# Optimization experiments

Hardware: AMD Instinct MI355X
Metric: run time of the kernel (lower is better)

## Reference

```python
import jax, jax.numpy as jnp
import numpy as np

B, T, D = 32, 512, 768
PROJ, HID, NL, VOCAB = 50, 409, 4, 17


def setup_inputs() -> dict:
    key = jax.random.key(0)
    ks = jax.random.split(key, 10)
    s = 0.05
    return {
        "enc": jax.random.normal(ks[0], (B, T, D), jnp.float32),
        "W_proj": jax.random.normal(ks[1], (PROJ, D), jnp.float32) * s,
        "Wih": jax.random.normal(ks[2], (NL, 2, 4 * HID, 2 * HID), jnp.float32) * s,
        "Whh": jax.random.normal(ks[3], (NL, 2, 4 * HID, HID), jnp.float32) * s,
        "bih": jax.random.normal(ks[4], (NL, 2, 4 * HID), jnp.float32) * s,
        "bhh": jax.random.normal(ks[5], (NL, 2, 4 * HID), jnp.float32) * s,
        "W1": jax.random.normal(ks[6], (512, 2 * HID), jnp.float32) * s,
        "b1": jax.random.normal(ks[7], (512,), jnp.float32) * s,
        "W2": jax.random.normal(ks[8], (VOCAB, 512), jnp.float32) * s,
        "b2": jax.random.normal(ks[9], (VOCAB,), jnp.float32) * s,
    }


def _ngram_pool(enc):
    # width-3 sliding mean; token 0 averages tokens [0:2]; last token is itself.
    b, t, d = enc.shape
    pad = jnp.pad(enc, ((0, 0), (1, 1), (0, 0)))
    ssum = pad[:, :-2] + pad[:, 1:-1] + pad[:, 2:]          # [B,T,D]
    cnt = jnp.full((t,), 3.0, enc.dtype).at[0].set(2.0)
    ng = ssum / cnt[None, :, None]
    return ng.at[:, -1].set(enc[:, -1])                      # last = mean of single token


def _lstm_dir(x, Wih, Whh, bih, bhh, reverse):
    # x: [T,B,in] -> hidden states [T,B,HID]; PyTorch gate order i,f,g,o.
    pre = jnp.einsum('tbi,gi->tbg', x, Wih) + bih + bhh     # [T,B,4H]
    bsz = x.shape[1]
    h0 = jnp.zeros((bsz, HID), x.dtype)

    def step(carry, p):
        h, c = carry
        g = p + h @ Whh.T
        i, f, gg, o = jnp.split(g, 4, axis=-1)
        c = jax.nn.sigmoid(f) * c + jax.nn.sigmoid(i) * jnp.tanh(gg)
        h = jax.nn.sigmoid(o) * jnp.tanh(c)
        return (h, c), h

    _, hs = jax.lax.scan(step, (h0, h0), pre, reverse=reverse)
    return hs


def reference(enc, W_proj, Wih, Whh, bih, bhh, W1, b1, W2, b2):
    ng = _ngram_pool(enc)                                    # [B,T,768]
    proj = ng @ W_proj.T                                     # [B,T,50]
    h = jnp.concatenate([enc, proj], axis=-1)                # [B,T,818]
    x = jnp.swapaxes(h, 0, 1)                                # [T,B,818]
    for l in range(NL):
        fwd = _lstm_dir(x, Wih[l, 0], Whh[l, 0], bih[l, 0], bhh[l, 0], False)
        bwd = _lstm_dir(x, Wih[l, 1], Whh[l, 1], bih[l, 1], bhh[l, 1], True)
        x = jnp.concatenate([fwd, bwd], axis=-1)             # [T,B,818]
    out = jnp.swapaxes(x, 0, 1)                              # [B,T,818]
    # fc: Linear -> Dropout(eval: identity) -> Linear
    logits = (out @ W1.T + b1) @ W2.T + b2                   # [B,T,17]
    return logits
```

## Files before the change

### kernel.cpp

```cpp
#include <hip/hip_runtime.h>
#include <stdint.h>


typedef __attribute__((ext_vector_type(8))) short bf16x8;
typedef __attribute__((ext_vector_type(4))) float f32x4;
typedef unsigned short u16;
typedef unsigned int u32;

constexpr int kT = 512, kB = 32, kDIN = 768, kPROJ = 50;
constexpr int kHID = 409, kKH = 416, kNG = 1664, kXD = 832;
constexpr int kM = kT * kB;
constexpr int kH4 = 1636;
constexpr int kIN = 818;

#define MFMA_B16(acc, a, b) \
  acc = __builtin_amdgcn_mfma_f32_16x16x32_bf16(a, b, acc, 0, 0, 0)

__device__ __forceinline__ u16 f2bf(float x) {
  uint32_t u = __float_as_uint(x);
  uint32_t r = (u + 0x7FFFu + ((u >> 16) & 1u)) >> 16;
  return (u16)r;
}
__device__ __forceinline__ float bf2f(u16 v) {
  return __uint_as_float(((uint32_t)v) << 16);
}
__device__ __forceinline__ float sigm(float x) { return 1.f / (1.f + __expf(-x)); }
__device__ __forceinline__ float tanh_(float x) { return 1.f - 2.f / (__expf(2.f * x) + 1.f); }

__device__ __forceinline__ void cload(bf16x8& d, const u16* p) {
  asm volatile("global_load_dwordx4 %0, %1, off sc0 sc1" : "=v"(d) : "v"(p) : "memory");
}
__device__ __forceinline__ u32 cload_u32(const u32* p) {
  u32 v;
  asm volatile("global_load_dword %0, %1, off sc0 sc1\n\ts_waitcnt vmcnt(0)"
               : "=v"(v) : "v"(p) : "memory");
  return v;
}
__device__ __forceinline__ void cstore_u32(u32* p, u32 v) {
  asm volatile("global_store_dword %0, %1, off sc0 sc1" :: "v"(p), "v"(v) : "memory");
}

__global__ void pack_wih_k(int layer, const float* __restrict__ Wsrc,
                           u16* __restrict__ wh, u16* __restrict__ wl) {
  const size_t total = (size_t)2 * kNG * kXD;
  for (size_t i = (size_t)blockIdx.x * blockDim.x + threadIdx.x; i < total;
       i += (size_t)gridDim.x * blockDim.x) {
    int k = (int)(i % kXD);
    size_t r1 = i / kXD;
    int row = (int)(r1 % kNG);
    int d = (int)(r1 / kNG);
    int g = row / kKH, j = row % kKH;
    float v = 0.f;
    if (j < kHID && k < kIN)
      v = Wsrc[((size_t)(layer * 2 + d) * kH4 + g * kHID + j) * kIN + k];
    u16 hb = f2bf(v);
    wh[i] = hb;
    wl[i] = f2bf(v - bf2f(hb));
  }
}

__global__ void pack_whh_k(int layer, const float* __restrict__ Wsrc,
                           u16* __restrict__ wh, u16* __restrict__ wl) {
  const size_t total = (size_t)2 * kNG * kKH;
  for (size_t i = (size_t)blockIdx.x * blockDim.x + threadIdx.x; i < total;
       i += (size_t)gridDim.x * blockDim.x) {
    int k = (int)(i % kKH);
    size_t r1 = i / kKH;
    int row = (int)(r1 % kNG);
    int d = (int)(r1 / kNG);
    int g = row / kKH, j = row % kKH;
    float v = 0.f;
    if (j < kHID && k < kHID)
      v = Wsrc[((size_t)(layer * 2 + d) * kH4 + g * kHID + j) * kHID + k];
    u16 hb = f2bf(v);
    wh[i] = hb;
    wl[i] = f2bf(v - bf2f(hb));
  }
}

__global__ void pack_bias_k(const float* __restrict__ bih,
                            const float* __restrict__ bhh,
                            float* __restrict__ bias) {
  int i = blockIdx.x * 256 + threadIdx.x;
  if (i >= 8 * kNG) return;
  int row = i % kNG, ld = i / kNG;
  int g = row / kKH, j = row % kKH;
  float v = 0.f;
  if (j < kHID) v = bih[ld * kH4 + g * kHID + j] + bhh[ld * kH4 + g * kHID + j];
  bias[i] = v;
}

__global__ void fold_fc_k(const float* __restrict__ W1, const float* __restrict__ b1,
                          const float* __restrict__ W2, const float* __restrict__ b2,
                          float* __restrict__ wfc, float* __restrict__ bfc) {
  int i = blockIdx.x * 256 + threadIdx.x;
  if (i >= 17 * kXD) return;
  int o = i / kXD, n = i % kXD;
  float s = 0.f;
  if (n < kIN) {
    for (int k = 0; k < 512; ++k) s += W2[o * 512 + k] * W1[(size_t)k * kIN + n];
  }
  wfc[i] = s;
  if (n == 0) {
    float bs = b2[o];
    for (int k = 0; k < 512; ++k) bs += W2[o * 512 + k] * b1[k];
    bfc[o] = bs;
  }
}

__global__ __launch_bounds__(256) void prep_k(const float* __restrict__ enc,
                                              const float* __restrict__ Wp,
                                              u16* __restrict__ x_h,
                                              u16* __restrict__ x_l,
                                              u16* __restrict__ y_h,
                                              u16* __restrict__ y_l) {
  const int t = blockIdx.x >> 2;
  const int b0 = (blockIdx.x & 3) * 8;
  const int tid = threadIdx.x;
  __shared__ __align__(16) float ng_s[8][kDIN];

  for (int idx = tid; idx < 8 * kDIN; idx += 256) {
    int bi = idx / kDIN, c = idx % kDIN;
    int b = b0 + bi;
    float e1 = enc[((size_t)b * kT + t) * kDIN + c];
    float ngv;
    if (t == 0)
      ngv = (e1 + enc[((size_t)b * kT + 1) * kDIN + c]) * 0.5f;
    else if (t == kT - 1)
      ngv = e1;
    else
      ngv = (enc[((size_t)b * kT + t - 1) * kDIN + c] + e1 +
             enc[((size_t)b * kT + t + 1) * kDIN + c]) * (1.f / 3.f);
    ng_s[bi][c] = ngv;
    size_t xo = ((size_t)t * kB + b) * kXD + c;
    u16 hb = f2bf(e1);
    x_h[xo] = hb;
    x_l[xo] = f2bf(e1 - bf2f(hb));
  }
  for (int idx = tid; idx < 8 * (kXD - kIN); idx += 256) {
    int bi = idx / (kXD - kIN), c = kIN + idx % (kXD - kIN);
    size_t xo = ((size_t)t * kB + b0 + bi) * kXD + c;
    x_h[xo] = 0; x_l[xo] = 0;
    y_h[xo] = 0; y_l[xo] = 0;
  }
  __syncthreads();

  const int w = tid >> 6, l_ = tid & 63;
  for (int p = w; p < kPROJ; p += 4) {
    float a0 = 0, a1 = 0, a2 = 0, a3 = 0, a4 = 0, a5 = 0, a6 = 0, a7 = 0;
    for (int j = l_; j < kDIN; j += 64) {
      float wv = Wp[(size_t)p * kDIN + j];
      a0 += wv * ng_s[0][j]; a1 += wv * ng_s[1][j];
      a2 += wv * ng_s[2][j]; a3 += wv * ng_s[3][j];
      a4 += wv * ng_s[4][j]; a5 += wv * ng_s[5][j];
      a6 += wv * ng_s[6][j]; a7 += wv * ng_s[7][j];
    }
    float acc8[8] = {a0, a1, a2, a3, a4, a5, a6, a7};
#pragma unroll
    for (int bi = 0; bi < 8; ++bi) {
      float v = acc8[bi];
      for (int off = 32; off > 0; off >>= 1) v += __shfl_down(v, off);
      if (l_ == 0) {
        size_t xo = ((size_t)t * kB + b0 + bi) * kXD + kDIN + p;
        u16 hb = f2bf(v);
        x_h[xo] = hb;
        x_l[xo] = f2bf(v - bf2f(hb));
      }
    }
  }
}

__global__ __launch_bounds__(256) void gemm_pre_k(
    const u16* __restrict__ Ah, const u16* __restrict__ Al,
    const u16* __restrict__ Bh, const u16* __restrict__ Bl,
    const float* __restrict__ bias, float* __restrict__ C,
    int m_base, int mtShift) {
  __shared__ __align__(16) u16 As_h[128 * 64], As_l[128 * 64];
  __shared__ __align__(16) u16 Bs_h[64 * 64], Bs_l[64 * 64];
  const int tid = threadIdx.x;
  const int l_ = tid & 63, w = tid >> 6;
  const int nt = blockIdx.x >> mtShift;
  const int mt = blockIdx.x & ((1 << mtShift) - 1);
  const int m0 = mt * 128, n0 = nt * 64;
  const int wr = (w & 1) * 64, wc = (w >> 1) * 32;

  f32x4 acc[4][2];
#pragma unroll
  for (int i = 0; i < 4; ++i)
#pragma unroll
    for (int j = 0; j < 2; ++j) acc[i][j] = f32x4{0.f, 0.f, 0.f, 0.f};

  for (int kt = 0; kt < 13; ++kt) {
    const int k0 = kt * 64;
#pragma unroll
    for (int i = 0; i < 4; ++i) {
      int ch = i * 256 + tid;
      int r = ch >> 3, kc = ch & 7;
      const size_t ga = (size_t)(m_base + m0 + r) * kXD + k0 + kc * 8;
      int dst = r * 64 + ((kc ^ (r & 7)) << 3);
      *(int4*)&As_h[dst] = *(const int4*)&Ah[ga];
      *(int4*)&As_l[dst] = *(const int4*)&Al[ga];
    }
#pragma unroll
    for (int i = 0; i < 2; ++i) {
      int ch = i * 256 + tid;
      int r = ch >> 3, kc = ch & 7;
      const size_t gb = (size_t)(n0 + r) * kXD + k0 + kc * 8;
      int dst = r * 64 + ((kc ^ (r & 7)) << 3);
      *(int4*)&Bs_h[dst] = *(const int4*)&Bh[gb];
      *(int4*)&Bs_l[dst] = *(const int4*)&Bl[gb];
    }
    __syncthreads();
#pragma unroll
    for (int ks = 0; ks < 2; ++ks) {
      bf16x8 a_h[4], a_l[4], b_h[2], b_l[2];
#pragma unroll
      for (int mi = 0; mi < 4; ++mi) {
        int r = wr + mi * 16 + (l_ & 15);
        int kc = ks * 4 + (l_ >> 4);
        int ad = r * 64 + ((kc ^ (r & 7)) << 3);
        a_h[mi] = *(const bf16x8*)&As_h[ad];
        a_l[mi] = *(const bf16x8*)&As_l[ad];
      }
#pragma unroll
      for (int ni = 0; ni < 2; ++ni) {
        int r = wc + ni * 16 + (l_ & 15);
        int kc = ks * 4 + (l_ >> 4);
        int ad = r * 64 + ((kc ^ (r & 7)) << 3);
        b_h[ni] = *(const bf16x8*)&Bs_h[ad];
        b_l[ni] = *(const bf16x8*)&Bs_l[ad];
      }
#pragma unroll
      for (int mi = 0; mi < 4; ++mi)
#pragma unroll
        for (int ni = 0; ni < 2; ++ni) {
          MFMA_B16(acc[mi][ni], a_h[mi], b_h[ni]);
          MFMA_B16(acc[mi][ni], a_h[mi], b_l[ni]);
          MFMA_B16(acc[mi][ni], a_l[mi], b_h[ni]);
        }
    }
    __syncthreads();
  }
#pragma unroll
  for (int mi = 0; mi < 4; ++mi)
#pragma unroll
    for (int ni = 0; ni < 2; ++ni) {
      int n = n0 + wc + ni * 16 + (l_ & 15);
      float bv = bias[n];
#pragma unroll
      for (int q = 0; q < 4; ++q) {
        int m = m0 + wr + mi * 16 + (l_ >> 4) * 4 + q;
        C[(size_t)m * kNG + n] = acc[mi][ni][q] + bv;
      }
    }
}

__global__ __launch_bounds__(256) void scan_k(
    int st0, int nsteps, const float* __restrict__ pre,
    const u16* __restrict__ whhH, const u16* __restrict__ whhL,
    u16* __restrict__ xo_h, u16* __restrict__ xo_l,
    u32* __restrict__ h_hi, u32* __restrict__ h_lo,
    float* __restrict__ c_glob, u32* __restrict__ layerFlags) {
  const int tid = threadIdx.x, l_ = tid & 63, w = tid >> 6;
  const int d = blockIdx.x & 1, s = blockIdx.x >> 1;
  const int mt = w & 1, nt2 = w >> 1;

  __shared__ __align__(16) u16 whh_s[2][64][424];
  __shared__ __align__(16) float gate_s[64][33];

  for (int idx = tid; idx < 64 * kKH; idx += 256) {
    int r = idx / kKH, k = idx % kKH;
    int g = r >> 4, j = r & 15;
    size_t src = ((size_t)d * kNG + g * kKH + s * 16 + j) * kKH + k;
    whh_s[0][r][k] = whhH[src];
    whh_s[1][r][k] = whhL[src];
  }

  const int ub = tid >> 3;
  const int uu = tid & 7;
  const int hid0 = s * 16 + 2 * uu;
  float c0 = 0.f, c1 = 0.f;
  if (st0 != 0) {
    c0 = c_glob[(d * 32 + ub) * kKH + hid0];
    c1 = c_glob[(d * 32 + ub) * kKH + hid0 + 1];
  }

  const int arow = mt * 16 + (l_ & 15);
  const int kq = (l_ >> 4) * 8;
  const int lr0 = nt2 * 32 + (l_ & 15);
  const int lr1 = nt2 * 32 + 16 + (l_ & 15);
  const int bq = mt * 16 + (l_ >> 4) * 4;
  const int n0g = (lr0 >> 4) * kKH + s * 16 + (lr0 & 15);
  const int n1g = (lr1 >> 4) * kKH + s * 16 + (lr1 & 15);
  const float* pre_d = pre + (size_t)d * ((size_t)nsteps * kB) * kNG;
  u32* flg = layerFlags + (size_t)d * kT * 32;

  __syncthreads();

  float preg[2][4];
  {
    int lt = d ? (nsteps - 1) : 0;
    const float* p = pre_d + ((size_t)lt * kB + bq) * kNG;
#pragma unroll
    for (int q = 0; q < 4; ++q) {
      preg[0][q] = p[(size_t)q * kNG + n0g];
      preg[1][q] = p[(size_t)q * kNG + n1g];
    }
  }

  for (int stl = 0; stl < nsteps; ++stl) {
    const int st = st0 + stl;
    const int teff = d ? (kT - 1 - st) : st;
    f32x4 acc0, acc1;
#pragma unroll
    for (int q = 0; q < 4; ++q) { acc0[q] = preg[0][q]; acc1[q] = preg[1][q]; }

    if (st > 0) {
      u32* fst = flg + (size_t)(st - 1) * 32;
      if (w == 0 && l_ < 26) {
        int guard = 0;
        while (cload_u32(fst + l_) == 0u) {
          __builtin_amdgcn_s_sleep(1);
          if (++guard > (1 << 20)) break;
        }
      }
      __syncthreads();
      const int slot = st & 1;
      const u16* hh = (const u16*)h_hi + (size_t)(slot * 2 + d) * kB * kKH;
      const u16* hl = (const u16*)h_lo + (size_t)(slot * 2 + d) * kB * kKH;
      bf16x8 ah[13], al[13];
#pragma unroll
      for (int ks = 0; ks < 13; ++ks) {
        cload(ah[ks], hh + arow * kKH + ks * 32 + kq);
        cload(al[ks], hl + arow * kKH + ks * 32 + kq);
      }
      asm volatile("s_waitcnt vmcnt(0)" ::: "memory");
      __builtin_amdgcn_sched_barrier(0);
#pragma unroll
      for (int ks = 0; ks < 13; ++ks) {
        bf16x8 bh0 = *(const bf16x8*)&whh_s[0][lr0][ks * 32 + kq];
        bf16x8 bl0 = *(const bf16x8*)&whh_s[1][lr0][ks * 32 + kq];
        bf16x8 bh1 = *(const bf16x8*)&whh_s[0][lr1][ks * 32 + kq];
        bf16x8 bl1 = *(const bf16x8*)&whh_s[1][lr1][ks * 32 + kq];
        MFMA_B16(acc0, ah[ks], bh0);
        MFMA_B16(acc0, ah[ks], bl0);
        MFMA_B16(acc0, al[ks], bh0);
        MFMA_B16(acc1, ah[ks], bh1);
        MFMA_B16(acc1, ah[ks], bl1);
        MFMA_B16(acc1, al[ks], bh1);
      }
    }

    if (stl + 1 < nsteps) {
      int lt = d ? (nsteps - 2 - stl) : (stl + 1);
      const float* p = pre_d + ((size_t)lt * kB + bq) * kNG;
#pragma unroll
      for (int q = 0; q < 4; ++q) {
        preg[0][q] = p[(size_t)q * kNG + n0g];
        preg[1][q] = p[(size_t)q * kNG + n1g];
      }
    }

#pragma unroll
    for (int q = 0; q < 4; ++q) {
      gate_s[lr0][bq + q] = acc0[q];
      gate_s[lr1][bq + q] = acc1[q];
    }
    __syncthreads();

    {
      int j0 = 2 * uu, j1 = 2 * uu + 1;
      float gi0 = gate_s[0 + j0][ub], gf0 = gate_s[16 + j0][ub];
      float gc0 = gate_s[32 + j0][ub], go0 = gate_s[48 + j0][ub];
      float gi1 = gate_s[0 + j1][ub], gf1 = gate_s[16 + j1][ub];
      float gc1 = gate_s[32 + j1][ub], go1 = gate_s[48 + j1][ub];
      c0 = sigm(gf0) * c0 + sigm(gi0) * tanh_(gc0);
      c1 = sigm(gf1) * c1 + sigm(gi1) * tanh_(gc1);
      float h0v = sigm(go0) * tanh_(c0);
      float h1v = sigm(go1) * tanh_(c1);

      u16 hb0 = f2bf(h0v), lb0 = f2bf(h0v - bf2f(hb0));
      u16 hb1 = f2bf(h1v), lb1 = f2bf(h1v - bf2f(hb1));
      const int outslot = (st + 1) & 1;
      u32 vh = (u32)hb0 | ((u32)hb1 << 16);
      u32 vl = (u32)lb0 | ((u32)lb1 << 16);
      size_t hw = ((size_t)(outslot * 2 + d) * kB + ub) * (kKH / 2) + (hid0 >> 1);
      cstore_u32(h_hi + hw, vh);
      cstore_u32(h_lo + hw, vl);
      if (hid0 < kHID) {
        size_t xo = ((size_t)teff * kB + ub) * kXD + d * kHID + hid0;
        xo_h[xo] = hb0;
        xo_l[xo] = lb0;
        if (hid0 + 1 < kHID) {
          xo_h[xo + 1] = hb1;
          xo_l[xo + 1] = lb1;
        }
      }
    }
    asm volatile("s_waitcnt vmcnt(0)" ::: "memory");
    __syncthreads();
    if (tid == 0) cstore_u32(flg + (size_t)st * 32 + s, 1u);
  }

  c_glob[(d * 32 + ub) * kKH + hid0] = c0;
  c_glob[(d * 32 + ub) * kKH + hid0 + 1] = c1;
}

__global__ __launch_bounds__(128) void fc_k(const u16* __restrict__ x_h,
                                            const u16* __restrict__ x_l,
                                            const float* __restrict__ wfc,
                                            const float* __restrict__ bfc,
                                            float* __restrict__ out) {
  const int m = blockIdx.x;
  const int t = m >> 5, b = m & 31;
  const int tid = threadIdx.x;
  __shared__ __align__(16) float xr[kXD];
  for (int i = tid; i < kXD; i += 128)
    xr[i] = bf2f(x_h[(size_t)m * kXD + i]) + bf2f(x_l[(size_t)m * kXD + i]);
  __syncthreads();
  const int w = tid >> 6, l_ = tid & 63;
  for (int o = w; o < 17; o += 2) {
    float acc = 0.f;
    for (int j = l_; j < kXD; j += 64) acc += xr[j] * wfc[(size_t)o * kXD + j];
    for (int off = 32; off > 0; off >>= 1) acc += __shfl_down(acc, off);
    if (l_ == 0) out[((size_t)b * kT + t) * 17 + o] = acc + bfc[o];
  }
}

extern "C" void kernel_launch(void* const* d_in, const int* in_sizes, int n_in,
                              void* d_out, int out_size, void* d_ws, size_t ws_size,
                              hipStream_t stream) {
  (void)in_sizes; (void)n_in; (void)out_size;
  const float* enc = (const float*)d_in[0];
  const float* Wp  = (const float*)d_in[1];
  const float* Wih = (const float*)d_in[2];
  const float* Whh = (const float*)d_in[3];
  const float* bih = (const float*)d_in[4];
  const float* bhh = (const float*)d_in[5];
  const float* W1  = (const float*)d_in[6];
  const float* b1  = (const float*)d_in[7];
  const float* W2  = (const float*)d_in[8];
  const float* b2  = (const float*)d_in[9];
  float* out = (float*)d_out;

  char* ws = (char*)d_ws;
  size_t off = 0;
  auto alloc = [&](size_t bytes) -> char* {
    char* p = ws + off;
    off += (bytes + 255) & ~(size_t)255;
    return p;
  };
  u16* x0_h  = (u16*)alloc((size_t)kM * kXD * 2);
  u16* x0_l  = (u16*)alloc((size_t)kM * kXD * 2);
  u16* x1_h  = (u16*)alloc((size_t)kM * kXD * 2);
  u16* x1_l  = (u16*)alloc((size_t)kM * kXD * 2);
  u16* wih_h = (u16*)alloc((size_t)2 * kNG * kXD * 2);
  u16* wih_l = (u16*)alloc((size_t)2 * kNG * kXD * 2);
  u16* whh_h = (u16*)alloc((size_t)2 * kNG * kKH * 2);
  u16* whh_l = (u16*)alloc((size_t)2 * kNG * kKH * 2);
  float* bias = (float*)alloc((size_t)8 * kNG * 4);
  u32* h_hi  = (u32*)alloc((size_t)2 * 2 * kB * kKH * 2);
  u32* h_lo  = (u32*)alloc((size_t)2 * 2 * kB * kKH * 2);
  float* c_glob = (float*)alloc((size_t)2 * kB * kKH * 4);
  u32* flags = (u32*)alloc((size_t)4 * 2 * kT * 32 * 4);
  float* wfc = (float*)alloc((size_t)17 * kXD * 4);
  float* bfc = (float*)alloc(32 * 4);

  int TC = 0;
  {
    const int cand[7] = {512, 256, 128, 64, 32, 16, 8};
    for (int i = 0; i < 7; ++i) {
      size_t preB = (size_t)2 * cand[i] * kB * kNG * 4;
      if (off + preB <= ws_size) { TC = cand[i]; break; }
    }
  }
  if (TC == 0) return;
  float* pre = (float*)alloc((size_t)2 * TC * kB * kNG * 4);
  const int mtShift = __builtin_ctz(TC / 4);
  const int nChunks = kT / TC;

  hipMemsetAsync(flags, 0, (size_t)4 * 2 * kT * 32 * 4, stream);

  pack_bias_k<<<dim3(52), dim3(256), 0, stream>>>(bih, bhh, bias);
  fold_fc_k<<<dim3(56), dim3(256), 0, stream>>>(W1, b1, W2, b2, wfc, bfc);
  prep_k<<<dim3(kT * 4), dim3(256), 0, stream>>>(enc, Wp, x0_h, x0_l, x1_h, x1_l);

  for (int l = 0; l < 4; ++l) {
    const bool even = (l & 1) == 0;
    const u16* xi_h = even ? x0_h : x1_h;
    const u16* xi_l = even ? x0_l : x1_l;
    u16* xo_h = even ? x1_h : x0_h;
    u16* xo_l = even ? x1_l : x0_l;

    pack_wih_k<<<dim3(2048), dim3(256), 0, stream>>>(l, Wih, wih_h, wih_l);
    pack_whh_k<<<dim3(1024), dim3(256), 0, stream>>>(l, Whh, whh_h, whh_l);
    for (int c = 0; c < nChunks; ++c) {
      const int st0 = c * TC;
      for (int dd = 0; dd < 2; ++dd) {
        const int m_base = (dd == 0 ? st0 : (kT - st0 - TC)) * kB;
        gemm_pre_k<<<dim3(26 << mtShift), dim3(256), 0, stream>>>(
            xi_h, xi_l, wih_h + (size_t)dd * kNG * kXD,
            wih_l + (size_t)dd * kNG * kXD, bias + (size_t)(l * 2 + dd) * kNG,
            pre + (size_t)dd * TC * kB * kNG, m_base, mtShift);
      }
      scan_k<<<dim3(52), dim3(256), 0, stream>>>(
          st0, TC, pre, whh_h, whh_l, xo_h, xo_l, h_hi, h_lo, c_glob,
          flags + (size_t)l * 2 * kT * 32);
    }
  }
  fc_k<<<dim3(kM), dim3(128), 0, stream>>>(x0_h, x0_l, wfc, bfc, out);
}
```

Baseline: 12.84 ms.

## Overlap h-state loads with MFMA and move non-critical stores off recurrence path

The recurrent LSTM step now waits on the h-state loads in three stages (vmcnt 18/8/0), so MFMAs on early k-slices start while later slices are still arriving. The x-output stores and the next-step preactivation prefetch move after the completion flag is published, which shortens the critical path between dependent steps. The spin-wait drops its s_sleep to cut polling latency, and the input-projection GEMM switches to direct global-to-LDS loads with the swizzle applied on the global side. In exchange, the spin loop polls harder, and the partial vmcnt waits rely on a particular load issue order.

```diff
diff --git a/kernel.cpp b/kernel.cpp
--- a/kernel.cpp
+++ b/kernel.cpp
@@ -38,6 +38,12 @@
 }
 __device__ __forceinline__ void cstore_u32(u32* p, u32 v) {
   asm volatile("global_store_dword %0, %1, off sc0 sc1" :: "v"(p), "v"(v) : "memory");
+}
+
+__device__ __forceinline__ void gload_lds16(const u16* g, u16* l) {
+  __builtin_amdgcn_global_load_lds(
+      (const __attribute__((address_space(1))) unsigned int*)g,
+      (__attribute__((address_space(3))) unsigned int*)l, 16, 0, 0);
 }
 
 __global__ void pack_wih_k(int layer, const float* __restrict__ Wsrc,
@@ -194,21 +200,21 @@
     const int k0 = kt * 64;
 #pragma unroll
     for (int i = 0; i < 4; ++i) {
-      int ch = i * 256 + tid;
-      int r = ch >> 3, kc = ch & 7;
-      const size_t ga = (size_t)(m_base + m0 + r) * kXD + k0 + kc * 8;
-      int dst = r * 64 + ((kc ^ (r & 7)) << 3);
-      *(int4*)&As_h[dst] = *(const int4*)&Ah[ga];
-      *(int4*)&As_l[dst] = *(const int4*)&Al[ga];
+      int slot = i * 256 + tid;
+      int r = slot >> 3, kc = slot & 7;
+      int kcs = kc ^ (r & 7);
+      const size_t ga = (size_t)(m_base + m0 + r) * kXD + k0 + kcs * 8;
+      gload_lds16(Ah + ga, &As_h[slot * 8]);
+      gload_lds16(Al + ga, &As_l[slot * 8]);
     }
 #pragma unroll
     for (int i = 0; i < 2; ++i) {
-      int ch = i * 256 + tid;
-      int r = ch >> 3, kc = ch & 7;
-      const size_t gb = (size_t)(n0 + r) * kXD + k0 + kc * 8;
-      int dst = r * 64 + ((kc ^ (r & 7)) << 3);
-      *(int4*)&Bs_h[dst] = *(const int4*)&Bh[gb];
-      *(int4*)&Bs_l[dst] = *(const int4*)&Bl[gb];
+      int slot = i * 256 + tid;
+      int r = slot >> 3, kc = slot & 7;
+      int kcs = kc ^ (r & 7);
+      const size_t gb = (size_t)(n0 + r) * kXD + k0 + kcs * 8;
+      gload_lds16(Bh + gb, &Bs_h[slot * 8]);
+      gload_lds16(Bl + gb, &Bs_l[slot * 8]);
     }
     __syncthreads();
 #pragma unroll
@@ -320,7 +326,6 @@
       if (w == 0 && l_ < 26) {
         int guard = 0;
         while (cload_u32(fst + l_) == 0u) {
-          __builtin_amdgcn_s_sleep(1);
           if (++guard > (1 << 20)) break;
         }
       }
@@ -334,10 +339,10 @@
         cload(ah[ks], hh + arow * kKH + ks * 32 + kq);
         cload(al[ks], hl + arow * kKH + ks * 32 + kq);
       }
-      asm volatile("s_waitcnt vmcnt(0)" ::: "memory");
+      asm volatile("s_waitcnt vmcnt(18)" ::: "memory");
       __builtin_amdgcn_sched_barrier(0);
 #pragma unroll
-      for (int ks = 0; ks < 13; ++ks) {
+      for (int ks = 0; ks < 4; ++ks) {
         bf16x8 bh0 = *(const bf16x8*)&whh_s[0][lr0][ks * 32 + kq];
         bf16x8 bl0 = *(const bf16x8*)&whh_s[1][lr0][ks * 32 + kq];
         bf16x8 bh1 = *(const bf16x8*)&whh_s[0][lr1][ks * 32 + kq];
@@ -349,15 +354,35 @@
         MFMA_B16(acc1, ah[ks], bl1);
         MFMA_B16(acc1, al[ks], bh1);
       }
-    }
-
-    if (stl + 1 < nsteps) {
-      int lt = d ? (nsteps - 2 - stl) : (stl + 1);
-      const float* p = pre_d + ((size_t)lt * kB + bq) * kNG;
-#pragma unroll
-      for (int q = 0; q < 4; ++q) {
-        preg[0][q] = p[(size_t)q * kNG + n0g];
-        preg[1][q] = p[(size_t)q * kNG + n1g];
+      asm volatile("s_waitcnt vmcnt(8)" ::: "memory");
+      __builtin_amdgcn_sched_barrier(0);
+#pragma unroll
+      for (int ks = 4; ks < 9; ++ks) {
+        bf16x8 bh0 = *(const bf16x8*)&whh_s[0][lr0][ks * 32 + kq];
+        bf16x8 bl0 = *(const bf16x8*)&whh_s[1][lr0][ks * 32 + kq];
+        bf16x8 bh1 = *(const bf16x8*)&whh_s[0][lr1][ks * 32 + kq];
+        bf16x8 bl1 = *(const bf16x8*)&whh_s[1][lr1][ks * 32 + kq];
+        MFMA_B16(acc0, ah[ks], bh0);
+        MFMA_B16(acc0, ah[ks], bl0);
+        MFMA_B16(acc0, al[ks], bh0);
+        MFMA_B16(acc1, ah[ks], bh1);
+        MFMA_B16(acc1, ah[ks], bl1);
+        MFMA_B16(acc1, al[ks], bh1);
+      }
+      asm volatile("s_waitcnt vmcnt(0)" ::: "memory");
+      __builtin_amdgcn_sched_barrier(0);
+#pragma unroll
+      for (int ks = 9; ks < 13; ++ks) {
+        bf16x8 bh0 = *(const bf16x8*)&whh_s[0][lr0][ks * 32 + kq];
+        bf16x8 bl0 = *(const bf16x8*)&whh_s[1][lr0][ks * 32 + kq];
+        bf16x8 bh1 = *(const bf16x8*)&whh_s[0][lr1][ks * 32 + kq];
+        bf16x8 bl1 = *(const bf16x8*)&whh_s[1][lr1][ks * 32 + kq];
+        MFMA_B16(acc0, ah[ks], bh0);
+        MFMA_B16(acc0, ah[ks], bl0);
+        MFMA_B16(acc0, al[ks], bh0);
+        MFMA_B16(acc1, ah[ks], bh1);
+        MFMA_B16(acc1, ah[ks], bl1);
+        MFMA_B16(acc1, al[ks], bh1);
       }
     }
 
@@ -368,6 +393,7 @@
     }
     __syncthreads();
 
+    u16 hb0, lb0, hb1, lb1;
     {
       int j0 = 2 * uu, j1 = 2 * uu + 1;
       float gi0 = gate_s[0 + j0][ub], gf0 = gate_s[16 + j0][ub];
@@ -379,27 +405,37 @@
       float h0v = sigm(go0) * tanh_(c0);
       float h1v = sigm(go1) * tanh_(c1);
 
-      u16 hb0 = f2bf(h0v), lb0 = f2bf(h0v - bf2f(hb0));
-      u16 hb1 = f2bf(h1v), lb1 = f2bf(h1v - bf2f(hb1));
+      hb0 = f2bf(h0v); lb0 = f2bf(h0v - bf2f(hb0));
+      hb1 = f2bf(h1v); lb1 = f2bf(h1v - bf2f(hb1));
       const int outslot = (st + 1) & 1;
       u32 vh = (u32)hb0 | ((u32)hb1 << 16);
       u32 vl = (u32)lb0 | ((u32)lb1 << 16);
       size_t hw = ((size_t)(outslot * 2 + d) * kB + ub) * (kKH / 2) + (hid0 >> 1);
       cstore_u32(h_hi + hw, vh);
       cstore_u32(h_lo + hw, vl);
-      if (hid0 < kHID) {
-        size_t xo = ((size_t)teff * kB + ub) * kXD + d * kHID + hid0;
-        xo_h[xo] = hb0;
-        xo_l[xo] = lb0;
-        if (hid0 + 1 < kHID) {
-          xo_h[xo + 1] = hb1;
-          xo_l[xo + 1] = lb1;
-        }
-      }
     }
     asm volatile("s_waitcnt vmcnt(0)" ::: "memory");
     __syncthreads();
     if (tid == 0) cstore_u32(flg + (size_t)st * 32 + s, 1u);
+
+    if (hid0 < kHID) {
+      size_t xo = ((size_t)teff * kB + ub) * kXD + d * kHID + hid0;
+      xo_h[xo] = hb0;
+      xo_l[xo] = lb0;
+      if (hid0 + 1 < kHID) {
+        xo_h[xo + 1] = hb1;
+        xo_l[xo + 1] = lb1;
+      }
+    }
+    if (stl + 1 < nsteps) {
+      int lt = d ? (nsteps - 2 - stl) : (stl + 1);
+      const float* p = pre_d + ((size_t)lt * kB + bq) * kNG;
+#pragma unroll
+      for (int q = 0; q < 4; ++q) {
+        preg[0][q] = p[(size_t)q * kNG + n0g];
+        preg[1][q] = p[(size_t)q * kNG + n1g];
+      }
+    }
   }
 
   c_glob[(d * 32 + ub) * kKH + hid0] = c0;
```

After: 11.15 ms. 13.2% less time.
